# Kernel optimization log

Hardware: AMD Instinct MI355X
Metric: run time of the kernel (lower is better)

Reference implementation:

```python
import jax, jax.numpy as jnp
import numpy as np

HIDDEN = 1024
HEADS = 16
D = HIDDEN // HEADS  # 64
RANK = 8
ALPHA = 16.0
SCALING = ALPHA / RANK  # LoRA scaling
SCALE = D ** (-0.5)


def _lora_proj(x, W, b, A, B):
    # x: [Bt,S,H]; W: [H,H] (out,in); A: [r,H]; B: [H,r]
    base = jnp.einsum('bsh,oh->bso', x, W) + b
    low = jnp.einsum('bsh,rh->bsr', x, A)
    return base + SCALING * jnp.einsum('bsr,or->bso', low, B)


def setup_inputs() -> dict:
    key = jax.random.key(0)
    ks = jax.random.split(key, 20)
    Bt, S = 2, 2048
    inp = {
        'q': jax.random.normal(ks[0], (Bt, S, HIDDEN), dtype=jnp.float32),
        'k': jax.random.normal(ks[1], (Bt, S, HIDDEN), dtype=jnp.float32),
        'v': jax.random.normal(ks[2], (Bt, S, HIDDEN), dtype=jnp.float32),
        'attn_bias': jax.random.normal(ks[3], (Bt, HEADS, S, S), dtype=jnp.float32),
    }
    sd = HIDDEN ** -0.5
    for i, name in enumerate(['q', 'k', 'v']):
        base = 4 + 4 * i
        inp[f'W{name}'] = jax.random.normal(ks[base + 0], (HIDDEN, HIDDEN), dtype=jnp.float32) * sd
        inp[f'b{name}'] = jnp.zeros((HIDDEN,), dtype=jnp.float32)
        inp[f'A{name}'] = jax.random.normal(ks[base + 1], (RANK, HIDDEN), dtype=jnp.float32) * sd
        inp[f'B{name}'] = jnp.zeros((HIDDEN, RANK), dtype=jnp.float32)
    return inp


def reference(q, k, v, attn_bias, Wq, bq, Aq, Bq, Wk, bk, Ak, Bk, Wv, bv, Av, Bv):
    Bt, S, _ = q.shape
    qh = _lora_proj(q, Wq, bq, Aq, Bq).reshape(Bt, S, HEADS, D)
    kh = _lora_proj(k, Wk, bk, Ak, Bk).reshape(Bt, S, HEADS, D)
    vh = _lora_proj(v, Wv, bv, Av, Bv).reshape(Bt, S, HEADS, D)
    scores = jnp.einsum('bqhd,bkhd->bhqk', qh * SCALE, kh) + attn_bias
    p = jax.nn.softmax(scores, axis=-1)  # dropout rate 0.0 -> identity
    out = jnp.einsum('bhqk,bkhd->bqhd', p, vh)
    return out.reshape(Bt, S, HEADS * D)
```

## Files before the change

### kernel.cpp

```cpp
#include <hip/hip_runtime.h>

#define SEQ 2048
#define HID 1024
#define NH 16
#define DH 64
#define BTCH 2
#define SCALE 0.125f
#define SCALING 2.0f

typedef __bf16 bf16;
typedef __attribute__((ext_vector_type(8))) __bf16 bf16x8;
typedef __attribute__((ext_vector_type(4))) float f32x4;

__device__ __forceinline__ f32x4 zero4() {
    f32x4 z; z[0] = 0.f; z[1] = 0.f; z[2] = 0.f; z[3] = 0.f; return z;
}

__global__ __launch_bounds__(256) void weff_kernel(
    const float* __restrict__ Wq, const float* __restrict__ Aq, const float* __restrict__ Bq,
    const float* __restrict__ Wk, const float* __restrict__ Ak, const float* __restrict__ Bk,
    const float* __restrict__ Wv, const float* __restrict__ Av, const float* __restrict__ Bv,
    bf16* __restrict__ weff)
{
    const int p = blockIdx.y;
    const float* W = (p == 0) ? Wq : (p == 1) ? Wk : Wv;
    const float* A = (p == 0) ? Aq : (p == 1) ? Ak : Av;
    const float* B = (p == 0) ? Bq : (p == 1) ? Bk : Bv;
    const int e = blockIdx.x * 256 + threadIdx.x;
    const int o = e >> 10;
    const int hc = e & 1023;
    float acc = W[e];
#pragma unroll
    for (int r = 0; r < 8; ++r)
        acc += SCALING * B[o * 8 + r] * A[r * 1024 + hc];
    weff[(size_t)p * 1024 * 1024 + e] = (bf16)acc;
}

__global__ __launch_bounds__(256) void proj_kernel(
    const float* __restrict__ xq, const float* __restrict__ xk, const float* __restrict__ xv,
    const float* __restrict__ bq, const float* __restrict__ bk, const float* __restrict__ bv,
    const bf16* __restrict__ weff, bf16* __restrict__ qkvh)
{
    __shared__ bf16 Xs[64 * 72];
    __shared__ bf16 Ws[64 * 72];

    const int p = blockIdx.z;
    const float* X    = (p == 0) ? xq : (p == 1) ? xk : xv;
    const float* bias = (p == 0) ? bq : (p == 1) ? bk : bv;
    const bf16* W = weff + (size_t)p * HID * HID;
    bf16* Y = qkvh + (size_t)p * BTCH * SEQ * HID;

    const int tid = threadIdx.x;
    const int wave = tid >> 6;
    const int lane = tid & 63;
    const int g = lane >> 4;
    const int lm = lane & 15;
    const int m0 = blockIdx.y * 64;
    const int n0 = blockIdx.x * 64;

    f32x4 acc[4];
#pragma unroll
    for (int c = 0; c < 4; ++c) acc[c] = zero4();

    for (int k0 = 0; k0 < HID; k0 += 64) {
#pragma unroll
        for (int i = 0; i < 2; ++i) {
            const int c = tid + i * 256;
            const int row = c >> 3;
            const int cv = c & 7;
            const float* xsrc = &X[(size_t)(m0 + row) * HID + k0 + cv * 8];
            f32x4 x0 = *(const f32x4*)(xsrc);
            f32x4 x1 = *(const f32x4*)(xsrc + 4);
            bf16x8 xb;
#pragma unroll
            for (int j = 0; j < 4; ++j) { xb[j] = (bf16)x0[j]; xb[4 + j] = (bf16)x1[j]; }
            *(bf16x8*)&Xs[row * 72 + cv * 8] = xb;
            *(bf16x8*)&Ws[row * 72 + cv * 8] =
                *(const bf16x8*)&W[(size_t)(n0 + row) * HID + k0 + cv * 8];
        }
        __syncthreads();
#pragma unroll
        for (int s = 0; s < 2; ++s) {
            bf16x8 a = *(const bf16x8*)&Xs[(wave * 16 + lm) * 72 + s * 32 + g * 8];
#pragma unroll
            for (int c = 0; c < 4; ++c) {
                bf16x8 bb = *(const bf16x8*)&Ws[(c * 16 + lm) * 72 + s * 32 + g * 8];
                acc[c] = __builtin_amdgcn_mfma_f32_16x16x32_bf16(a, bb, acc[c], 0, 0, 0);
            }
        }
        __syncthreads();
    }

#pragma unroll
    for (int c = 0; c < 4; ++c) {
        const float bv_ = bias[n0 + c * 16 + lm];
#pragma unroll
        for (int r = 0; r < 4; ++r) {
            const int row = m0 + wave * 16 + g * 4 + r;
            Y[(size_t)row * HID + n0 + c * 16 + lm] = (bf16)(acc[c][r] + bv_);
        }
    }
}

__global__ __launch_bounds__(256) void attn_kernel(
    const bf16* __restrict__ qkvh, const float* __restrict__ attn_bias,
    float* __restrict__ out)
{
    __shared__ bf16 Ks[64 * 72];
    __shared__ bf16 Vt[64 * 72];
    __shared__ bf16 Ps[64 * 72];

    const int tid = threadIdx.x;
    const int wave = tid >> 6;
    const int lane = tid & 63;
    const int g = lane >> 4;
    const int lm = lane & 15;

    const int q0 = blockIdx.x * 64;
    const int h = blockIdx.y;
    const int b = blockIdx.z;

    const bf16* qh = qkvh;
    const bf16* kh = qkvh + (size_t)BTCH * SEQ * HID;
    const bf16* vh = qkvh + (size_t)2 * BTCH * SEQ * HID;

    const bf16* qrow = qh + (size_t)(b * SEQ + q0 + wave * 16 + lm) * HID + h * DH;
    bf16x8 qf0 = *(const bf16x8*)(qrow + g * 8);
    bf16x8 qf1 = *(const bf16x8*)(qrow + 32 + g * 8);

    f32x4 acc_o[4];
    float m2[4], l[4];
#pragma unroll
    for (int c = 0; c < 4; ++c) acc_o[c] = zero4();
#pragma unroll
    for (int r = 0; r < 4; ++r) { m2[r] = -__builtin_inff(); l[r] = 0.f; }

    const size_t bias_base = (size_t)(b * NH + h) * SEQ * SEQ;

    for (int kv0 = 0; kv0 < SEQ; kv0 += 64) {
#pragma unroll
        for (int i = 0; i < 2; ++i) {
            const int c = tid + i * 256;
            const int row = c >> 3;
            const int cv = c & 7;
            const size_t src = (size_t)(b * SEQ + kv0 + row) * HID + h * DH + cv * 8;
            *(bf16x8*)&Ks[row * 72 + cv * 8] = *(const bf16x8*)&kh[src];
            bf16x8 vv = *(const bf16x8*)&vh[src];
#pragma unroll
            for (int j = 0; j < 8; ++j)
                Vt[(cv * 8 + j) * 72 + row] = vv[j];
        }
        __syncthreads();

        f32x4 sacc[4];
#pragma unroll
        for (int c = 0; c < 4; ++c) sacc[c] = zero4();
#pragma unroll
        for (int s = 0; s < 2; ++s) {
            bf16x8 a = (s == 0) ? qf0 : qf1;
#pragma unroll
            for (int c = 0; c < 4; ++c) {
                bf16x8 bb = *(const bf16x8*)&Ks[(c * 16 + lm) * 72 + s * 32 + g * 8];
                sacc[c] = __builtin_amdgcn_mfma_f32_16x16x32_bf16(a, bb, sacc[c], 0, 0, 0);
            }
        }

        float t[4][4];
#pragma unroll
        for (int c = 0; c < 4; ++c) {
#pragma unroll
            for (int r = 0; r < 4; ++r) {
                const int qq = q0 + wave * 16 + g * 4 + r;
                const int kk = kv0 + c * 16 + lm;
                const float bval = attn_bias[bias_base + (size_t)qq * SEQ + kk];
                t[c][r] = sacc[c][r] * SCALE + bval;
            }
        }

        float rmax[4];
#pragma unroll
        for (int r = 0; r < 4; ++r)
            rmax[r] = fmaxf(fmaxf(t[0][r], t[1][r]), fmaxf(t[2][r], t[3][r]));
#pragma unroll
        for (int off = 1; off < 16; off <<= 1) {
#pragma unroll
            for (int r = 0; r < 4; ++r)
                rmax[r] = fmaxf(rmax[r], __shfl_xor(rmax[r], off));
        }

        float alpha[4];
#pragma unroll
        for (int r = 0; r < 4; ++r) {
            const float mn = fmaxf(m2[r], rmax[r]);
            alpha[r] = __expf(m2[r] - mn);
            m2[r] = mn;
        }

        float rsum[4] = {0.f, 0.f, 0.f, 0.f};
#pragma unroll
        for (int c = 0; c < 4; ++c) {
#pragma unroll
            for (int r = 0; r < 4; ++r) {
                const float pv = __expf(t[c][r] - m2[r]);
                rsum[r] += pv;
                Ps[(wave * 16 + g * 4 + r) * 72 + c * 16 + lm] = (bf16)pv;
            }
        }
#pragma unroll
        for (int off = 1; off < 16; off <<= 1) {
#pragma unroll
            for (int r = 0; r < 4; ++r)
                rsum[r] += __shfl_xor(rsum[r], off);
        }
#pragma unroll
        for (int r = 0; r < 4; ++r)
            l[r] = l[r] * alpha[r] + rsum[r];
#pragma unroll
        for (int c = 0; c < 4; ++c) {
#pragma unroll
            for (int r = 0; r < 4; ++r)
                acc_o[c][r] *= alpha[r];
        }

        __syncthreads();

#pragma unroll
        for (int s = 0; s < 2; ++s) {
            bf16x8 pa = *(const bf16x8*)&Ps[(wave * 16 + lm) * 72 + s * 32 + g * 8];
#pragma unroll
            for (int c = 0; c < 4; ++c) {
                bf16x8 vb = *(const bf16x8*)&Vt[(c * 16 + lm) * 72 + s * 32 + g * 8];
                acc_o[c] = __builtin_amdgcn_mfma_f32_16x16x32_bf16(pa, vb, acc_o[c], 0, 0, 0);
            }
        }
        __syncthreads();
    }

#pragma unroll
    for (int c = 0; c < 4; ++c) {
#pragma unroll
        for (int r = 0; r < 4; ++r) {
            const int qq = q0 + wave * 16 + g * 4 + r;
            out[(size_t)(b * SEQ + qq) * HID + h * DH + c * 16 + lm] =
                acc_o[c][r] / l[r];
        }
    }
}

extern "C" void kernel_launch(void* const* d_in, const int* in_sizes, int n_in,
                              void* d_out, int out_size, void* d_ws, size_t ws_size,
                              hipStream_t stream)
{
    const float* q  = (const float*)d_in[0];
    const float* k  = (const float*)d_in[1];
    const float* v  = (const float*)d_in[2];
    const float* ab = (const float*)d_in[3];
    const float* Wq = (const float*)d_in[4];
    const float* bq = (const float*)d_in[5];
    const float* Aq = (const float*)d_in[6];
    const float* Bq = (const float*)d_in[7];
    const float* Wk = (const float*)d_in[8];
    const float* bk = (const float*)d_in[9];
    const float* Ak = (const float*)d_in[10];
    const float* Bk = (const float*)d_in[11];
    const float* Wv = (const float*)d_in[12];
    const float* bv = (const float*)d_in[13];
    const float* Av = (const float*)d_in[14];
    const float* Bv = (const float*)d_in[15];

    bf16* weff = (bf16*)d_ws;
    bf16* qkvh = weff + (size_t)3 * 1024 * 1024;

    weff_kernel<<<dim3(1024 * 1024 / 256, 3), 256, 0, stream>>>(
        Wq, Aq, Bq, Wk, Ak, Bk, Wv, Av, Bv, weff);

    proj_kernel<<<dim3(HID / 64, BTCH * SEQ / 64, 3), 256, 0, stream>>>(
        q, k, v, bq, bk, bv, weff, qkvh);

    attn_kernel<<<dim3(SEQ / 64, NH, BTCH), 256, 0, stream>>>(
        qkvh, ab, (float*)d_out);
}
```

Baseline: 894.4 us.

## Pre-cast inputs, enlarge projection tiles, pre-transpose V, use exp2 softmax

Adds a separate kernel that casts the fp32 inputs to bf16, and grows the projection GEMM tile from 64x64 to 128x128 with a 4x4 MFMA block per wave for more register reuse. V is transposed by its own kernel so the attention loop loads V tiles as vectors instead of doing scalar scattered LDS writes. The softmax scale and log2(e) are folded into the Q projection so the attention kernel can use exp2 with one FMA on the bias. The cost is two extra launches and extra workspace traffic for the bf16 copies and the transposed V.

```diff
diff --git a/kernel.cpp b/kernel.cpp
--- a/kernel.cpp
+++ b/kernel.cpp
@@ -7,6 +7,7 @@
 #define BTCH 2
 #define SCALE 0.125f
 #define SCALING 2.0f
+#define LOG2E 1.4426950408889634f
 
 typedef __bf16 bf16;
 typedef __attribute__((ext_vector_type(8))) __bf16 bf16x8;
@@ -36,16 +37,31 @@
     weff[(size_t)p * 1024 * 1024 + e] = (bf16)acc;
 }
 
+__global__ __launch_bounds__(256) void cast_kernel(
+    const float* __restrict__ xq, const float* __restrict__ xk, const float* __restrict__ xv,
+    bf16* __restrict__ xb)
+{
+    const int p = blockIdx.y;
+    const float* X = (p == 0) ? xq : (p == 1) ? xk : xv;
+    const size_t e = ((size_t)blockIdx.x * 256 + threadIdx.x) * 8;
+    f32x4 x0 = *(const f32x4*)(X + e);
+    f32x4 x1 = *(const f32x4*)(X + e + 4);
+    bf16x8 xo;
+#pragma unroll
+    for (int j = 0; j < 4; ++j) { xo[j] = (bf16)x0[j]; xo[4 + j] = (bf16)x1[j]; }
+    *(bf16x8*)&xb[(size_t)p * BTCH * SEQ * HID + e] = xo;
+}
+
 __global__ __launch_bounds__(256) void proj_kernel(
-    const float* __restrict__ xq, const float* __restrict__ xk, const float* __restrict__ xv,
+    const bf16* __restrict__ xb,
     const float* __restrict__ bq, const float* __restrict__ bk, const float* __restrict__ bv,
     const bf16* __restrict__ weff, bf16* __restrict__ qkvh)
 {
-    __shared__ bf16 Xs[64 * 72];
-    __shared__ bf16 Ws[64 * 72];
+    __shared__ bf16 Xs[128 * 72];
+    __shared__ bf16 Ws[128 * 72];
 
     const int p = blockIdx.z;
-    const float* X    = (p == 0) ? xq : (p == 1) ? xk : xv;
+    const bf16* X = xb + (size_t)p * BTCH * SEQ * HID;
     const float* bias = (p == 0) ? bq : (p == 1) ? bk : bv;
     const bf16* W = weff + (size_t)p * HID * HID;
     bf16* Y = qkvh + (size_t)p * BTCH * SEQ * HID;
@@ -55,56 +71,98 @@
     const int lane = tid & 63;
     const int g = lane >> 4;
     const int lm = lane & 15;
-    const int m0 = blockIdx.y * 64;
-    const int n0 = blockIdx.x * 64;
-
-    f32x4 acc[4];
-#pragma unroll
-    for (int c = 0; c < 4; ++c) acc[c] = zero4();
+    const int wm = (wave >> 1) * 64;
+    const int wn = (wave & 1) * 64;
+    const int m0 = blockIdx.y * 128;
+    const int n0 = blockIdx.x * 128;
+
+    f32x4 acc[4][4];
+#pragma unroll
+    for (int mi = 0; mi < 4; ++mi)
+#pragma unroll
+        for (int ni = 0; ni < 4; ++ni) acc[mi][ni] = zero4();
 
     for (int k0 = 0; k0 < HID; k0 += 64) {
 #pragma unroll
-        for (int i = 0; i < 2; ++i) {
-            const int c = tid + i * 256;
-            const int row = c >> 3;
-            const int cv = c & 7;
-            const float* xsrc = &X[(size_t)(m0 + row) * HID + k0 + cv * 8];
-            f32x4 x0 = *(const f32x4*)(xsrc);
-            f32x4 x1 = *(const f32x4*)(xsrc + 4);
-            bf16x8 xb;
-#pragma unroll
-            for (int j = 0; j < 4; ++j) { xb[j] = (bf16)x0[j]; xb[4 + j] = (bf16)x1[j]; }
-            *(bf16x8*)&Xs[row * 72 + cv * 8] = xb;
-            *(bf16x8*)&Ws[row * 72 + cv * 8] =
-                *(const bf16x8*)&W[(size_t)(n0 + row) * HID + k0 + cv * 8];
+        for (int i = 0; i < 4; ++i) {
+            const int idx = tid + i * 256;
+            const int row = idx >> 3;
+            const int ch = idx & 7;
+            *(bf16x8*)&Xs[row * 72 + ch * 8] =
+                *(const bf16x8*)&X[(size_t)(m0 + row) * HID + k0 + ch * 8];
+            *(bf16x8*)&Ws[row * 72 + ch * 8] =
+                *(const bf16x8*)&W[(size_t)(n0 + row) * HID + k0 + ch * 8];
         }
         __syncthreads();
 #pragma unroll
         for (int s = 0; s < 2; ++s) {
-            bf16x8 a = *(const bf16x8*)&Xs[(wave * 16 + lm) * 72 + s * 32 + g * 8];
-#pragma unroll
-            for (int c = 0; c < 4; ++c) {
-                bf16x8 bb = *(const bf16x8*)&Ws[(c * 16 + lm) * 72 + s * 32 + g * 8];
-                acc[c] = __builtin_amdgcn_mfma_f32_16x16x32_bf16(a, bb, acc[c], 0, 0, 0);
-            }
-        }
-        __syncthreads();
-    }
-
-#pragma unroll
-    for (int c = 0; c < 4; ++c) {
-        const float bv_ = bias[n0 + c * 16 + lm];
-#pragma unroll
-        for (int r = 0; r < 4; ++r) {
-            const int row = m0 + wave * 16 + g * 4 + r;
-            Y[(size_t)row * HID + n0 + c * 16 + lm] = (bf16)(acc[c][r] + bv_);
-        }
+            bf16x8 a[4], b[4];
+#pragma unroll
+            for (int mi = 0; mi < 4; ++mi)
+                a[mi] = *(const bf16x8*)&Xs[(wm + mi * 16 + lm) * 72 + s * 32 + g * 8];
+#pragma unroll
+            for (int ni = 0; ni < 4; ++ni)
+                b[ni] = *(const bf16x8*)&Ws[(wn + ni * 16 + lm) * 72 + s * 32 + g * 8];
+#pragma unroll
+            for (int mi = 0; mi < 4; ++mi)
+#pragma unroll
+                for (int ni = 0; ni < 4; ++ni)
+                    acc[mi][ni] = __builtin_amdgcn_mfma_f32_16x16x32_bf16(
+                        a[mi], b[ni], acc[mi][ni], 0, 0, 0);
+        }
+        __syncthreads();
+    }
+
+    const float oscale = (p == 0) ? (SCALE * LOG2E) : 1.0f;
+#pragma unroll
+    for (int ni = 0; ni < 4; ++ni) {
+        const float bv_ = bias[n0 + wn + ni * 16 + lm];
+#pragma unroll
+        for (int mi = 0; mi < 4; ++mi) {
+#pragma unroll
+            for (int r = 0; r < 4; ++r) {
+                const int row = m0 + wm + mi * 16 + g * 4 + r;
+                Y[(size_t)row * HID + n0 + wn + ni * 16 + lm] =
+                    (bf16)((acc[mi][ni][r] + bv_) * oscale);
+            }
+        }
+    }
+}
+
+__global__ __launch_bounds__(256) void vtrans_kernel(
+    const bf16* __restrict__ vh, bf16* __restrict__ vt)
+{
+    __shared__ bf16 T[64 * 76];
+    const int tid = threadIdx.x;
+    const int s0 = blockIdx.x * 64;
+    const int c0 = blockIdx.y * 64;
+    const int b = blockIdx.z;
+
+#pragma unroll
+    for (int i = 0; i < 2; ++i) {
+        const int idx = tid + i * 256;
+        const int row = idx >> 3;
+        const int ch = idx & 7;
+        *(bf16x8*)&T[row * 76 + ch * 8] =
+            *(const bf16x8*)&vh[(size_t)(b * SEQ + s0 + row) * HID + c0 + ch * 8];
+    }
+    __syncthreads();
+#pragma unroll
+    for (int i = 0; i < 2; ++i) {
+        const int idx = tid + i * 256;
+        const int row = idx >> 3;
+        const int ch = idx & 7;
+        bf16x8 o;
+#pragma unroll
+        for (int u = 0; u < 8; ++u)
+            o[u] = T[(ch * 8 + u) * 76 + row];
+        *(bf16x8*)&vt[((size_t)b * HID + c0 + row) * SEQ + s0 + ch * 8] = o;
     }
 }
 
 __global__ __launch_bounds__(256) void attn_kernel(
-    const bf16* __restrict__ qkvh, const float* __restrict__ attn_bias,
-    float* __restrict__ out)
+    const bf16* __restrict__ qkvh, const bf16* __restrict__ vt,
+    const float* __restrict__ attn_bias, float* __restrict__ out)
 {
     __shared__ bf16 Ks[64 * 72];
     __shared__ bf16 Vt[64 * 72];
@@ -122,7 +180,6 @@
 
     const bf16* qh = qkvh;
     const bf16* kh = qkvh + (size_t)BTCH * SEQ * HID;
-    const bf16* vh = qkvh + (size_t)2 * BTCH * SEQ * HID;
 
     const bf16* qrow = qh + (size_t)(b * SEQ + q0 + wave * 16 + lm) * HID + h * DH;
     bf16x8 qf0 = *(const bf16x8*)(qrow + g * 8);
@@ -140,15 +197,13 @@
     for (int kv0 = 0; kv0 < SEQ; kv0 += 64) {
 #pragma unroll
         for (int i = 0; i < 2; ++i) {
-            const int c = tid + i * 256;
-            const int row = c >> 3;
-            const int cv = c & 7;
-            const size_t src = (size_t)(b * SEQ + kv0 + row) * HID + h * DH + cv * 8;
-            *(bf16x8*)&Ks[row * 72 + cv * 8] = *(const bf16x8*)&kh[src];
-            bf16x8 vv = *(const bf16x8*)&vh[src];
-#pragma unroll
-            for (int j = 0; j < 8; ++j)
-                Vt[(cv * 8 + j) * 72 + row] = vv[j];
+            const int idx = tid + i * 256;
+            const int row = idx >> 3;
+            const int ch = idx & 7;
+            *(bf16x8*)&Ks[row * 72 + ch * 8] =
+                *(const bf16x8*)&kh[(size_t)(b * SEQ + kv0 + row) * HID + h * DH + ch * 8];
+            *(bf16x8*)&Vt[row * 72 + ch * 8] =
+                *(const bf16x8*)&vt[((size_t)b * HID + h * DH + row) * SEQ + kv0 + ch * 8];
         }
         __syncthreads();
 
@@ -173,7 +228,7 @@
                 const int qq = q0 + wave * 16 + g * 4 + r;
                 const int kk = kv0 + c * 16 + lm;
                 const float bval = attn_bias[bias_base + (size_t)qq * SEQ + kk];
-                t[c][r] = sacc[c][r] * SCALE + bval;
+                t[c][r] = __builtin_fmaf(bval, LOG2E, sacc[c][r]);
             }
         }
 
@@ -192,7 +247,7 @@
 #pragma unroll
         for (int r = 0; r < 4; ++r) {
             const float mn = fmaxf(m2[r], rmax[r]);
-            alpha[r] = __expf(m2[r] - mn);
+            alpha[r] = exp2f(m2[r] - mn);
             m2[r] = mn;
         }
 
@@ -201,7 +256,7 @@
         for (int c = 0; c < 4; ++c) {
 #pragma unroll
             for (int r = 0; r < 4; ++r) {
-                const float pv = __expf(t[c][r] - m2[r]);
+                const float pv = exp2f(t[c][r] - m2[r]);
                 rsum[r] += pv;
                 Ps[(wave * 16 + g * 4 + r) * 72 + c * 16 + lm] = (bf16)pv;
             }
@@ -270,13 +325,20 @@
 
     bf16* weff = (bf16*)d_ws;
     bf16* qkvh = weff + (size_t)3 * 1024 * 1024;
-
-    weff_kernel<<<dim3(1024 * 1024 / 256, 3), 256, 0, stream>>>(
+    bf16* xb   = qkvh + (size_t)3 * BTCH * SEQ * HID;
+    bf16* vtb  = xb   + (size_t)3 * BTCH * SEQ * HID;
+
+    weff_kernel<<<dim3(4096, 3), 256, 0, stream>>>(
         Wq, Aq, Bq, Wk, Ak, Bk, Wv, Av, Bv, weff);
 
-    proj_kernel<<<dim3(HID / 64, BTCH * SEQ / 64, 3), 256, 0, stream>>>(
-        q, k, v, bq, bk, bv, weff, qkvh);
+    cast_kernel<<<dim3(2048, 3), 256, 0, stream>>>(q, k, v, xb);
+
+    proj_kernel<<<dim3(HID / 128, BTCH * SEQ / 128, 3), 256, 0, stream>>>(
+        xb, bq, bk, bv, weff, qkvh);
+
+    vtrans_kernel<<<dim3(SEQ / 64, HID / 64, BTCH), 256, 0, stream>>>(
+        qkvh + (size_t)2 * BTCH * SEQ * HID, vtb);
 
     attn_kernel<<<dim3(SEQ / 64, NH, BTCH), 256, 0, stream>>>(
-        qkvh, ab, (float*)d_out);
-}
+        qkvh, vtb, ab, (float*)d_out);
+}
```

After: 849.3 us. -5.0%, faster.
